# Kernel tuning notes

Measured on AMD Instinct MI355X. Metric: run time of the kernel, lower is better.

## Reference

```python
import jax, jax.numpy as jnp
import numpy as np

B = 8
N = 1024


def _sqrtm_psd(P):
    # symmetric PSD matrix square root via eigendecomposition
    w, V = jnp.linalg.eigh(P)
    return (V * jnp.sqrt(jnp.clip(w, 0.0))) @ V.T


def setup_inputs() -> dict:
    key = jax.random.key(0)
    k1, k2, k3 = jax.random.split(key, 3)
    x = jax.random.normal(k1, (1, B, N, 1), dtype=jnp.float32)
    # PSD covariance with nonnegative entries so abs() is a no-op and sqrtm is real
    A = jax.random.uniform(k2, (N, N), dtype=jnp.float32)
    P_u = (A @ A.T) / N
    Q_k = jax.random.uniform(k3, (N, N), dtype=jnp.float32)
    return {"x": x, "P_u": P_u, "Q_k": Q_k}


def reference(x, P_u, Q_k):
    n = x.shape[2]  # N
    # sigma = x.repeat(1,1,1,N): [1,B,N,N]
    sigma0 = jnp.broadcast_to(x, (1, x.shape[1], n, n))
    # p = sqrtm(N * |P_u|)
    p = _sqrtm_psd(n * jnp.abs(P_u))
    # concat(sigma+p, sigma-p) along last dim -> [1,B,N,2N]
    sigma = jnp.concatenate((sigma0 + p, sigma0 - p), axis=3)
    scale = 1.0 / (2 * n)
    x_bar = jnp.mean(sigma, axis=3)  # [1,B,N]
    # Faithful to original: only sigma[0,0] is used for the deviations,
    # while the mean varies with the batch index i2.
    points = sigma[0, 0]  # [N, 2N]
    c = points[None, :, :] - x_bar[0][:, :, None]  # [B, N, 2N]
    S = jnp.einsum('bni,bmi->bnm', c, c)  # sum of 2N outer products per batch
    P_k = S * scale + (Q_k ** 2) * 0.01
    return P_k, jnp.transpose(sigma, (0, 1, 3, 2))


if __name__ == "__main__":
    out = reference(**setup_inputs())
    print(out[0].shape, out[1].shape)
```

## Files before the change

kernel.cpp:

```cpp
#include <hip/hip_runtime.h>
#include <math.h>

#define NN 1024
#define BB 8
#define NS_ITERS 10
#define EPS_SHIFT 4.0f
#define MB (1u<<20)

typedef __attribute__((ext_vector_type(8))) short short8;
typedef __attribute__((ext_vector_type(4))) float floatx4;

__device__ __forceinline__ ushort f2bf(float f) {
    union { float f; uint32_t u; } v; v.f = f;
    uint32_t u = v.u;
    uint32_t r = (u + 0x7fffu + ((u >> 16) & 1u)) >> 16;
    return (ushort)r;
}
__device__ __forceinline__ float bf2f(ushort h) {
    union { uint32_t u; float f; } v; v.u = ((uint32_t)h) << 16;
    return v.f;
}

__device__ __forceinline__ void gload16(const ushort* g, ushort* s) {
    __builtin_amdgcn_global_load_lds(
        (__attribute__((address_space(1))) unsigned int*)(g),
        (__attribute__((address_space(3))) unsigned int*)(s), 16, 0, 0);
}

__device__ __forceinline__ float block_sum(float v) {
    #pragma unroll
    for (int off = 32; off > 0; off >>= 1) v += __shfl_down(v, off, 64);
    __shared__ float red[4];
    int lane = threadIdx.x & 63, wid = threadIdx.x >> 6;
    if (lane == 0) red[wid] = v;
    __syncthreads();
    float t = 0.f;
    if (threadIdx.x == 0) t = red[0] + red[1] + red[2] + red[3];
    return t;
}

__global__ __launch_bounds__(256) void matvec_abs(const float* __restrict__ pu,
                                                  const float* __restrict__ x,
                                                  float* __restrict__ y,
                                                  int use_ones) {
    int row = blockIdx.x;
    const float4* pr = (const float4*)(pu + (size_t)row * NN);
    float4 p = pr[threadIdx.x];
    float s;
    if (use_ones) {
        s = fabsf(p.x) + fabsf(p.y) + fabsf(p.z) + fabsf(p.w);
    } else {
        float4 xx = ((const float4*)x)[threadIdx.x];
        s = fabsf(p.x) * xx.x + fabsf(p.y) * xx.y + fabsf(p.z) * xx.z + fabsf(p.w) * xx.w;
    }
    s = block_sum(s);
    if (threadIdx.x == 0) y[row] = s;
}

__global__ void norm_vec(const float* __restrict__ y, float* __restrict__ v) {
    float ss = 0.f;
    for (int i = threadIdx.x; i < NN; i += 256) { float t = y[i]; ss += t * t; }
    #pragma unroll
    for (int off = 32; off > 0; off >>= 1) ss += __shfl_down(ss, off, 64);
    __shared__ float red[4];
    __shared__ float s_inv;
    int lane = threadIdx.x & 63, wid = threadIdx.x >> 6;
    if (lane == 0) red[wid] = ss;
    __syncthreads();
    if (threadIdx.x == 0) s_inv = rsqrtf(red[0] + red[1] + red[2] + red[3]);
    __syncthreads();
    float inv = s_inv;
    for (int i = threadIdx.x; i < NN; i += 256) v[i] = y[i] * inv;
}

__global__ void dot_vec(const float* __restrict__ a, const float* __restrict__ b,
                        float* __restrict__ out) {
    float s = 0.f;
    for (int i = threadIdx.x; i < NN; i += 256) s += a[i] * b[i];
    s = block_sum(s);
    if (threadIdx.x == 0) out[0] = s;
}

__global__ __launch_bounds__(256) void deflate_kernel(const float* __restrict__ pu,
                                                      const float* __restrict__ v,
                                                      const float* __restrict__ w,
                                                      float* __restrict__ sc,
                                                      float* __restrict__ D) {
    int idx = blockIdx.x * 256 + threadIdx.x;
    int row = idx >> 8;
    int c0 = (idx & 255) << 2;
    float lam = sc[5];
    float vr = v[row], wr = w[row];
    float4 p = ((const float4*)pu)[idx];
    float4 vc = *(const float4*)(v + c0);
    float4 wc = *(const float4*)(w + c0);
    float4 d;
    d.x = (float)NN * (fabsf(p.x) - vr * wc.x - wr * vc.x + lam * vr * vc.x);
    d.y = (float)NN * (fabsf(p.y) - vr * wc.y - wr * vc.y + lam * vr * vc.y);
    d.z = (float)NN * (fabsf(p.z) - vr * wc.z - wr * vc.z + lam * vr * vc.z);
    d.w = (float)NN * (fabsf(p.w) - vr * wc.w - wr * vc.w + lam * vr * vc.w);
    int dd = row - c0;
    if (dd == 0) d.x += EPS_SHIFT;
    else if (dd == 1) d.y += EPS_SHIFT;
    else if (dd == 2) d.z += EPS_SHIFT;
    else if (dd == 3) d.w += EPS_SHIFT;
    ((float4*)D)[idx] = d;
    float ss = d.x * d.x + d.y * d.y + d.z * d.z + d.w * d.w;
    ss = block_sum(ss);
    if (threadIdx.x == 0) atomicAdd(sc, ss);
}

__global__ void finalize_kernel(float* sc) {
    float c = sqrtf(sc[0]);
    sc[1] = 1.f / c;
    sc[2] = sqrtf(c);
    sc[4] = sqrtf((float)NN * sc[5]);
}

__device__ __forceinline__ void tile_swizzle64(int& row0, int& col0, int& zz) {
    int f = blockIdx.x + (blockIdx.y << 4) + (blockIdx.z << 8);
    int p = f & 7;
    int i = f >> 3;
    if (gridDim.z == 2) {
        zz = p & 1;
        int s = p >> 1;
        row0 = (((s >> 1) << 3) + (i >> 3)) << 6;
        col0 = (((s & 1) << 3) + (i & 7)) << 6;
    } else {
        zz = 0;
        row0 = (((p >> 1) << 2) + (i >> 3)) << 6;
        col0 = (((p & 1) << 3) + (i & 7)) << 6;
    }
}

__device__ __forceinline__ void mm_dev(const ushort* __restrict__ Ah,
                                       const ushort* __restrict__ Al,
                                       const ushort* __restrict__ Bh,
                                       const ushort* __restrict__ Bl,
                                       int row0, int col0, int kb, int kc,
                                       float* __restrict__ Cf,
                                       float* __restrict__ CfT,
                                       ushort* __restrict__ Chi,
                                       ushort* __restrict__ Clo) {
    __shared__ __align__(16) ushort lds[4 * 4 * 2048];
    const int t = threadIdx.x;
    const int w = t >> 6, l = t & 63;
    const int fm = l & 15, fq = l >> 4;
    const int lrow = l >> 2;
    const int lcol = (l & 3) << 3;

    const ushort* gh = w ? Bh : Ah;
    const ushort* gl = w ? Bl : Al;
    const int r0 = w ? col0 : row0;
    const ushort* ghp = gh + (size_t)(r0 + lrow) * NN + kb + lcol;
    const ushort* glp = gl + (size_t)(r0 + lrow) * NN + kb + lcol;

    floatx4 acc[4][2];
    #pragma unroll
    for (int mi = 0; mi < 4; ++mi) {
        acc[mi][0] = (floatx4)0.f;
        acc[mi][1] = (floatx4)0.f;
    }

    auto STAGE = [&](int bufi, int kt) {
        const int koff = kt << 5;
        ushort* sb = lds + (bufi << 13) + (w << 12);
        #pragma unroll
        for (int rb = 0; rb < 4; ++rb) {
            gload16(ghp + (size_t)(rb << 4) * NN + koff, sb + (rb << 9));
            gload16(glp + (size_t)(rb << 4) * NN + koff, sb + 2048 + (rb << 9));
        }
    };

    auto COMPUTE = [&](int bufi) {
        const ushort* Ash = lds + (bufi << 13);
        const ushort* Asl = Ash + 2048;
        const ushort* Bsh = Ash + 4096;
        const ushort* Bsl = Ash + 6144;
        const int bo = ((w << 5) + fm) * 32 + (fq << 3);
        short8 bh0 = *(const short8*)&Bsh[bo];
        short8 bh1 = *(const short8*)&Bsh[bo + 512];
        short8 bl0 = *(const short8*)&Bsl[bo];
        short8 bl1 = *(const short8*)&Bsl[bo + 512];
        #pragma unroll
        for (int mi = 0; mi < 4; ++mi) {
            const int ao = ((mi << 4) + fm) * 32 + (fq << 3);
            short8 ah = *(const short8*)&Ash[ao];
            short8 al = *(const short8*)&Asl[ao];
            acc[mi][0] = __builtin_amdgcn_mfma_f32_16x16x32_bf16(ah, bh0, acc[mi][0], 0, 0, 0);
            acc[mi][1] = __builtin_amdgcn_mfma_f32_16x16x32_bf16(ah, bh1, acc[mi][1], 0, 0, 0);
            acc[mi][0] = __builtin_amdgcn_mfma_f32_16x16x32_bf16(al, bh0, acc[mi][0], 0, 0, 0);
            acc[mi][1] = __builtin_amdgcn_mfma_f32_16x16x32_bf16(al, bh1, acc[mi][1], 0, 0, 0);
            acc[mi][0] = __builtin_amdgcn_mfma_f32_16x16x32_bf16(ah, bl0, acc[mi][0], 0, 0, 0);
            acc[mi][1] = __builtin_amdgcn_mfma_f32_16x16x32_bf16(ah, bl1, acc[mi][1], 0, 0, 0);
        }
    };

    const int nk = kc >> 5;
    STAGE(0, 0);
    STAGE(1, 1);
    STAGE(2, 2);
    #pragma unroll 1
    for (int kt = 0; kt < nk; ++kt) {
        if (kt + 2 < nk)       asm volatile("s_waitcnt vmcnt(16)" ::: "memory");
        else if (kt + 1 < nk)  asm volatile("s_waitcnt vmcnt(8)"  ::: "memory");
        else                   asm volatile("s_waitcnt vmcnt(0)"  ::: "memory");
        __builtin_amdgcn_s_barrier();
        __builtin_amdgcn_sched_barrier(0);
        if (kt + 3 < nk) STAGE((kt + 3) & 3, kt + 3);
        COMPUTE(kt & 3);
    }

    #pragma unroll
    for (int mi = 0; mi < 4; ++mi) {
        #pragma unroll
        for (int r = 0; r < 4; ++r) {
            int row = row0 + (mi << 4) + (fq << 2) + r;
            #pragma unroll
            for (int ni = 0; ni < 2; ++ni) {
                int col = col0 + (w << 5) + (ni << 4) + fm;
                float v = acc[mi][ni][r];
                size_t idx = (size_t)row * NN + col;
                if (Cf) {
                    Cf[idx] = v;
                } else {
                    ushort h = f2bf(v);
                    Chi[idx] = h;
                    Clo[idx] = f2bf(v - bf2f(h));
                }
            }
        }
    }

    if (CfT) {
        __syncthreads();
        float* lf = (float*)lds;
        #pragma unroll
        for (int mi = 0; mi < 4; ++mi) {
            #pragma unroll
            for (int r = 0; r < 4; ++r) {
                int rl = (mi << 4) + (fq << 2) + r;
                #pragma unroll
                for (int ni = 0; ni < 2; ++ni) {
                    int cl = (w << 5) + (ni << 4) + fm;
                    lf[cl * 68 + rl] = acc[mi][ni][r];
                }
            }
        }
        __syncthreads();
        int c = t >> 1, half = t & 1;
        const float* src = lf + c * 68 + (half << 5);
        float* dst = CfT + (size_t)(col0 + c) * NN + row0 + (half << 5);
        #pragma unroll
        for (int j = 0; j < 8; ++j)
            *(float4*)(dst + (j << 2)) = *(const float4*)(src + (j << 2));
    }
}

__global__ __launch_bounds__(128) void k_stage1(const ushort* __restrict__ Zh,
                                                const ushort* __restrict__ Zl,
                                                const ushort* __restrict__ Yh,
                                                const ushort* __restrict__ Yl,
                                                float* __restrict__ Mp,
                                                float* __restrict__ MpT0,
                                                float* __restrict__ MpT1) {
    int row0, col0, s;
    tile_swizzle64(row0, col0, s);
    mm_dev(Zh, Zl, Yh, Yl, row0, col0,
           s * (NN / 2), NN / 2, Mp + (size_t)s * NN * NN,
           s ? MpT1 : MpT0, nullptr, nullptr);
}

__global__ __launch_bounds__(128) void k_stage2(const ushort* __restrict__ Yh,
                                                const ushort* __restrict__ Yl,
                                                const ushort* __restrict__ Wh,
                                                const ushort* __restrict__ Wl,
                                                const ushort* __restrict__ Zh,
                                                const ushort* __restrict__ Zl,
                                                ushort* __restrict__ Ynh,
                                                ushort* __restrict__ Ynl,
                                                ushort* __restrict__ Znh,
                                                ushort* __restrict__ Znl) {
    int row0, col0, zz;
    tile_swizzle64(row0, col0, zz);
    if (zz == 0)
        mm_dev(Yh, Yl, Wh, Wl, row0, col0, 0, NN,
               nullptr, nullptr, Ynh, Ynl);
    else
        mm_dev(Wh, Wl, Zh, Zl, row0, col0, 0, NN,
               nullptr, nullptr, Znh, Znl);
}

__global__ __launch_bounds__(128) void k_final(const ushort* __restrict__ Yh,
                                               const ushort* __restrict__ Yl,
                                               const ushort* __restrict__ Wh,
                                               const ushort* __restrict__ Wl,
                                               float* __restrict__ Yf,
                                               float* __restrict__ YfT) {
    int row0, col0, zz;
    tile_swizzle64(row0, col0, zz);
    mm_dev(Yh, Yl, Wh, Wl, row0, col0, 0, NN,
           Yf, YfT, nullptr, nullptr);
}

__global__ __launch_bounds__(256) void k_wsplit(const float* __restrict__ Mp,
                                                const float* __restrict__ MpT0,
                                                const float* __restrict__ MpT1,
                                                ushort* __restrict__ Wh,
                                                ushort* __restrict__ Wl) {
    int i = blockIdx.x * 256 + threadIdx.x;
    int row = i >> 8, c0 = (i & 255) << 2;
    float4 m0 = ((const float4*)Mp)[i];
    float4 m1 = ((const float4*)Mp)[i + NN * NN / 4];
    float4 t0 = ((const float4*)MpT0)[i];
    float4 t1 = ((const float4*)MpT1)[i];
    float wv[4] = {-0.25f * (m0.x + m1.x + t0.x + t1.x),
                   -0.25f * (m0.y + m1.y + t0.y + t1.y),
                   -0.25f * (m0.z + m1.z + t0.z + t1.z),
                   -0.25f * (m0.w + m1.w + t0.w + t1.w)};
    int dd = row - c0;
    if (dd >= 0 && dd < 4) wv[dd] += 1.5f;
    ushort4 hv, lv;
    ushort* hp = (ushort*)&hv; ushort* lp = (ushort*)&lv;
    #pragma unroll
    for (int j = 0; j < 4; ++j) {
        ushort h = f2bf(wv[j]); hp[j] = h; lp[j] = f2bf(wv[j] - bf2f(h));
    }
    *(ushort4*)&Wh[(size_t)i << 2] = hv;
    *(ushort4*)&Wl[(size_t)i << 2] = lv;
}

__global__ __launch_bounds__(256) void k_wsplit0(const float* __restrict__ D,
                                                 const float* __restrict__ sc,
                                                 ushort* __restrict__ Yh,
                                                 ushort* __restrict__ Yl,
                                                 ushort* __restrict__ Wh,
                                                 ushort* __restrict__ Wl) {
    int i = blockIdx.x * 256 + threadIdx.x;
    int row = i >> 8, c0 = (i & 255) << 2;
    float invc = sc[1];
    float4 d = ((const float4*)D)[i];
    float yv[4] = {d.x * invc, d.y * invc, d.z * invc, d.w * invc};
    ushort4 yh, yl, wh, wl;
    ushort* yhp = (ushort*)&yh; ushort* ylp = (ushort*)&yl;
    ushort* whp = (ushort*)&wh; ushort* wlp = (ushort*)&wl;
    int dd = row - c0;
    #pragma unroll
    for (int j = 0; j < 4; ++j) {
        float y = yv[j];
        ushort h = f2bf(y); yhp[j] = h; ylp[j] = f2bf(y - bf2f(h));
        float wv = ((dd == j) ? 1.5f : 0.f) - 0.5f * y;
        ushort h2 = f2bf(wv); whp[j] = h2; wlp[j] = f2bf(wv - bf2f(h2));
    }
    *(ushort4*)&Yh[(size_t)i << 2] = yh;
    *(ushort4*)&Yl[(size_t)i << 2] = yl;
    *(ushort4*)&Wh[(size_t)i << 2] = wh;
    *(ushort4*)&Wl[(size_t)i << 2] = wl;
}

__global__ __launch_bounds__(256) void out0_kernel(const float* __restrict__ x,
                                                   const float* __restrict__ pu,
                                                   const float* __restrict__ qk,
                                                   float* __restrict__ out) {
    int i = blockIdx.x * blockDim.x + threadIdx.x;
    int rem = i & (NN * NN / 4 - 1);
    int b = i >> 18;
    int n = rem >> 8;
    int m4 = (rem & 255) << 2;
    float dn = x[n] - x[b * NN + n];
    float4 x0v = *(const float4*)(x + m4);
    float4 xbv = *(const float4*)(x + b * NN + m4);
    float4 pv = ((const float4*)pu)[rem];
    float4 qv = ((const float4*)qk)[rem];
    float4 o;
    o.x = dn * (x0v.x - xbv.x) + fabsf(pv.x) + 0.01f * qv.x * qv.x;
    o.y = dn * (x0v.y - xbv.y) + fabsf(pv.y) + 0.01f * qv.y * qv.y;
    o.z = dn * (x0v.z - xbv.z) + fabsf(pv.z) + 0.01f * qv.z * qv.z;
    o.w = dn * (x0v.w - xbv.w) + fabsf(pv.w) + 0.01f * qv.w * qv.w;
    ((float4*)out)[i] = o;
}

__global__ __launch_bounds__(256) void k_out1(const float* __restrict__ x,
                                              const float* __restrict__ Yf,
                                              const float* __restrict__ YfT,
                                              const float* __restrict__ sc,
                                              const float* __restrict__ v,
                                              float* __restrict__ out1) {
    int i = blockIdx.x * 256 + threadIdx.x;
    int j = i >> 8, i0 = (i & 255) << 2;
    float s = 0.5f * sc[2], s1v = sc[4] * v[j];
    float4 yr = *(const float4*)(Yf + (size_t)j * NN + i0);
    float4 yc = *(const float4*)(YfT + (size_t)j * NN + i0);
    float4 vc = *(const float4*)(v + i0);
    float4 p;
    p.x = s * (yr.x + yc.x) + s1v * vc.x;
    p.y = s * (yr.y + yc.y) + s1v * vc.y;
    p.z = s * (yr.z + yc.z) + s1v * vc.z;
    p.w = s * (yr.w + yc.w) + s1v * vc.w;
    #pragma unroll
    for (int b = 0; b < BB; ++b) {
        float4 xv = *(const float4*)(x + b * NN + i0);
        float4 a, m;
        a.x = xv.x + p.x; a.y = xv.y + p.y; a.z = xv.z + p.z; a.w = xv.w + p.w;
        m.x = xv.x - p.x; m.y = xv.y - p.y; m.z = xv.z - p.z; m.w = xv.w - p.w;
        float* base = out1 + (size_t)b * 2 * NN * NN;
        *(float4*)(base + (size_t)j * NN + i0) = a;
        *(float4*)(base + (size_t)(NN + j) * NN + i0) = m;
    }
}

extern "C" void kernel_launch(void* const* d_in, const int* in_sizes, int n_in,
                              void* d_out, int out_size, void* d_ws, size_t ws_size,
                              hipStream_t stream) {
    const float* x  = (const float*)d_in[0];
    const float* pu = (const float*)d_in[1];
    const float* qk = (const float*)d_in[2];
    float* out = (float*)d_out;
    char* ws = (char*)d_ws;

    float* Mp = (float*)ws;
    float* D  = Mp;
    float* Yf = Mp;
    float* YfT = (float*)(ws + (size_t)4 * MB);
    ushort* hi[5]; ushort* lo[5];
    for (int k = 0; k < 5; ++k) {
        hi[k] = (ushort*)(ws + (size_t)8 * MB + (size_t)k * 4 * MB);
        lo[k] = (ushort*)(ws + (size_t)8 * MB + (size_t)k * 4 * MB + 2 * MB);
    }
    float* vv = (float*)(ws + (size_t)28 * MB);
    float* vw = (float*)(ws + (size_t)28 * MB + 4096);
    float* vt = (float*)(ws + (size_t)28 * MB + 8192);
    float* sc = (float*)(ws + (size_t)28 * MB + 12288);

    hipMemsetAsync(sc, 0, 64, stream);
    matvec_abs<<<NN, 256, 0, stream>>>(pu, vv, vt, 1);
    norm_vec<<<1, 256, 0, stream>>>(vt, vv);
    matvec_abs<<<NN, 256, 0, stream>>>(pu, vv, vt, 0);
    norm_vec<<<1, 256, 0, stream>>>(vt, vv);
    matvec_abs<<<NN, 256, 0, stream>>>(pu, vv, vw, 0);
    dot_vec<<<1, 256, 0, stream>>>(vv, vw, sc + 5);
    deflate_kernel<<<NN * NN / 4 / 256, 256, 0, stream>>>(pu, vv, vw, sc, D);
    finalize_kernel<<<1, 1, 0, stream>>>(sc);

    k_wsplit0<<<NN * NN / 4 / 256, 256, 0, stream>>>(D, sc, hi[0], lo[0], hi[1], lo[1]);
    k_stage2<<<dim3(16, 16, 1), 128, 0, stream>>>(hi[0], lo[0], hi[1], lo[1],
                                                  hi[0], lo[0],
                                                  hi[2], lo[2], hi[3], lo[3]);
    int Y = 2, Z = 1, f0 = 0, f1 = 3, f2 = 4;

    for (int it = 1; it < NS_ITERS; ++it) {
        int W = f0;
        float* MpT0 = (float*)hi[f1];
        float* MpT1 = (float*)hi[f2];
        k_stage1<<<dim3(16, 16, 2), 128, 0, stream>>>(hi[Z], lo[Z], hi[Y], lo[Y],
                                                      Mp, MpT0, MpT1);
        k_wsplit<<<NN * NN / 4 / 256, 256, 0, stream>>>(Mp, MpT0, MpT1,
                                                        hi[W], lo[W]);
        if (it + 1 < NS_ITERS) {
            int Yn = f1, Zn = f2;
            k_stage2<<<dim3(16, 16, 2), 128, 0, stream>>>(
                hi[Y], lo[Y], hi[W], lo[W], hi[Z], lo[Z],
                hi[Yn], lo[Yn], hi[Zn], lo[Zn]);
            f0 = Y; f1 = Z; f2 = W;
            Y = Yn; Z = Zn;
        } else {
            k_final<<<dim3(16, 16, 1), 128, 0, stream>>>(hi[Y], lo[Y], hi[W], lo[W],
                                                         Yf, YfT);
        }
    }

    out0_kernel<<<(BB * NN * NN / 4) / 256, 256, 0, stream>>>(x, pu, qk, out);
    k_out1<<<NN * NN / 4 / 256, 256, 0, stream>>>(x, Yf, YfT, sc, vv,
                                                  out + (size_t)BB * NN * NN);
}
```

Before: 569.3 us.

## Split K across the two waves in the tile GEMM and reduce through LDS

The 64x64 tile GEMM used to split the output columns between its two waves, with both waves sharing every staged K-slice behind a block barrier. Now each wave computes the full 64x64 tile over alternating K-slices with its own private staging and no per-iteration barrier, and the two partial sums are added through LDS at the end. This removes the per-step s_barrier and lets each wave pipeline on its own. In exchange each wave holds twice as many accumulators, needs more registers, and adds an LDS reduction epilogue, which may lower occupancy.

```diff
diff --git a/kernel.cpp b/kernel.cpp
--- a/kernel.cpp
+++ b/kernel.cpp
@@ -142,83 +142,107 @@
                                        float* __restrict__ CfT,
                                        ushort* __restrict__ Chi,
                                        ushort* __restrict__ Clo) {
-    __shared__ __align__(16) ushort lds[4 * 4 * 2048];
+    __shared__ __align__(16) ushort lds[4 * 8192];
     const int t = threadIdx.x;
     const int w = t >> 6, l = t & 63;
     const int fm = l & 15, fq = l >> 4;
     const int lrow = l >> 2;
     const int lcol = (l & 3) << 3;
 
-    const ushort* gh = w ? Bh : Ah;
-    const ushort* gl = w ? Bl : Al;
-    const int r0 = w ? col0 : row0;
-    const ushort* ghp = gh + (size_t)(r0 + lrow) * NN + kb + lcol;
-    const ushort* glp = gl + (size_t)(r0 + lrow) * NN + kb + lcol;
-
-    floatx4 acc[4][2];
-    #pragma unroll
-    for (int mi = 0; mi < 4; ++mi) {
-        acc[mi][0] = (floatx4)0.f;
-        acc[mi][1] = (floatx4)0.f;
-    }
-
-    auto STAGE = [&](int bufi, int kt) {
+    const ushort* Ahp = Ah + (size_t)(row0 + lrow) * NN + kb + lcol;
+    const ushort* Alp = Al + (size_t)(row0 + lrow) * NN + kb + lcol;
+    const ushort* Bhp = Bh + (size_t)(col0 + lrow) * NN + kb + lcol;
+    const ushort* Blp = Bl + (size_t)(col0 + lrow) * NN + kb + lcol;
+
+    floatx4 acc[4][4];
+    #pragma unroll
+    for (int mi = 0; mi < 4; ++mi)
+        #pragma unroll
+        for (int ni = 0; ni < 4; ++ni) acc[mi][ni] = (floatx4)0.f;
+
+    auto STAGE = [&](int kt) {
         const int koff = kt << 5;
-        ushort* sb = lds + (bufi << 13) + (w << 12);
+        ushort* sb = lds + ((kt & 3) << 13);
         #pragma unroll
         for (int rb = 0; rb < 4; ++rb) {
-            gload16(ghp + (size_t)(rb << 4) * NN + koff, sb + (rb << 9));
-            gload16(glp + (size_t)(rb << 4) * NN + koff, sb + 2048 + (rb << 9));
+            gload16(Ahp + (size_t)(rb << 4) * NN + koff, sb + (rb << 9));
+            gload16(Alp + (size_t)(rb << 4) * NN + koff, sb + 2048 + (rb << 9));
+            gload16(Bhp + (size_t)(rb << 4) * NN + koff, sb + 4096 + (rb << 9));
+            gload16(Blp + (size_t)(rb << 4) * NN + koff, sb + 6144 + (rb << 9));
         }
     };
 
-    auto COMPUTE = [&](int bufi) {
-        const ushort* Ash = lds + (bufi << 13);
+    const int nk = kc >> 5;
+    STAGE(w);
+    STAGE(w + 2);
+    #pragma unroll 1
+    for (int kt = w; kt < nk; kt += 2) {
+        if (kt + 2 < nk) asm volatile("s_waitcnt vmcnt(16)" ::: "memory");
+        else             asm volatile("s_waitcnt vmcnt(0)"  ::: "memory");
+        __builtin_amdgcn_sched_barrier(0);
+        const ushort* Ash = lds + ((kt & 3) << 13);
         const ushort* Asl = Ash + 2048;
         const ushort* Bsh = Ash + 4096;
         const ushort* Bsl = Ash + 6144;
-        const int bo = ((w << 5) + fm) * 32 + (fq << 3);
-        short8 bh0 = *(const short8*)&Bsh[bo];
-        short8 bh1 = *(const short8*)&Bsh[bo + 512];
-        short8 bl0 = *(const short8*)&Bsl[bo];
-        short8 bl1 = *(const short8*)&Bsl[bo + 512];
-        #pragma unroll
-        for (int mi = 0; mi < 4; ++mi) {
-            const int ao = ((mi << 4) + fm) * 32 + (fq << 3);
-            short8 ah = *(const short8*)&Ash[ao];
-            short8 al = *(const short8*)&Asl[ao];
-            acc[mi][0] = __builtin_amdgcn_mfma_f32_16x16x32_bf16(ah, bh0, acc[mi][0], 0, 0, 0);
-            acc[mi][1] = __builtin_amdgcn_mfma_f32_16x16x32_bf16(ah, bh1, acc[mi][1], 0, 0, 0);
-            acc[mi][0] = __builtin_amdgcn_mfma_f32_16x16x32_bf16(al, bh0, acc[mi][0], 0, 0, 0);
-            acc[mi][1] = __builtin_amdgcn_mfma_f32_16x16x32_bf16(al, bh1, acc[mi][1], 0, 0, 0);
-            acc[mi][0] = __builtin_amdgcn_mfma_f32_16x16x32_bf16(ah, bl0, acc[mi][0], 0, 0, 0);
-            acc[mi][1] = __builtin_amdgcn_mfma_f32_16x16x32_bf16(ah, bl1, acc[mi][1], 0, 0, 0);
+        short8 ah[4], al[4], bh[4], bl[4];
+        #pragma unroll
+        for (int i = 0; i < 4; ++i) {
+            const int ro = ((i << 4) + fm) * 32 + (fq << 3);
+            ah[i] = *(const short8*)&Ash[ro];
+            al[i] = *(const short8*)&Asl[ro];
+            bh[i] = *(const short8*)&Bsh[ro];
+            bl[i] = *(const short8*)&Bsl[ro];
         }
-    };
-
-    const int nk = kc >> 5;
-    STAGE(0, 0);
-    STAGE(1, 1);
-    STAGE(2, 2);
-    #pragma unroll 1
-    for (int kt = 0; kt < nk; ++kt) {
-        if (kt + 2 < nk)       asm volatile("s_waitcnt vmcnt(16)" ::: "memory");
-        else if (kt + 1 < nk)  asm volatile("s_waitcnt vmcnt(8)"  ::: "memory");
-        else                   asm volatile("s_waitcnt vmcnt(0)"  ::: "memory");
-        __builtin_amdgcn_s_barrier();
+        asm volatile("s_waitcnt lgkmcnt(0)" ::: "memory");
         __builtin_amdgcn_sched_barrier(0);
-        if (kt + 3 < nk) STAGE((kt + 3) & 3, kt + 3);
-        COMPUTE(kt & 3);
-    }
-
-    #pragma unroll
-    for (int mi = 0; mi < 4; ++mi) {
+        if (kt + 4 < nk) STAGE(kt + 4);
+        #pragma unroll
+        for (int mi = 0; mi < 4; ++mi)
+            #pragma unroll
+            for (int ni = 0; ni < 4; ++ni) {
+                acc[mi][ni] = __builtin_amdgcn_mfma_f32_16x16x32_bf16(ah[mi], bh[ni], acc[mi][ni], 0, 0, 0);
+                acc[mi][ni] = __builtin_amdgcn_mfma_f32_16x16x32_bf16(al[mi], bh[ni], acc[mi][ni], 0, 0, 0);
+                acc[mi][ni] = __builtin_amdgcn_mfma_f32_16x16x32_bf16(ah[mi], bl[ni], acc[mi][ni], 0, 0, 0);
+            }
+    }
+
+    __syncthreads();
+    float* lf = (float*)lds;
+    const int dep0 = w ? 0 : 2;
+    const int own0 = w ? 2 : 0;
+    #pragma unroll
+    for (int m2 = 0; m2 < 2; ++m2) {
+        #pragma unroll
+        for (int ni = 0; ni < 4; ++ni)
+            #pragma unroll
+            for (int r = 0; r < 4; ++r) {
+                int row = ((dep0 + m2) << 4) + (fq << 2) + r;
+                int col = (ni << 4) + fm;
+                lf[row * 66 + col] = acc[dep0 + m2][ni][r];
+            }
+    }
+    __syncthreads();
+    #pragma unroll
+    for (int m2 = 0; m2 < 2; ++m2) {
+        #pragma unroll
+        for (int ni = 0; ni < 4; ++ni)
+            #pragma unroll
+            for (int r = 0; r < 4; ++r) {
+                int row = ((own0 + m2) << 4) + (fq << 2) + r;
+                int col = (ni << 4) + fm;
+                acc[own0 + m2][ni][r] += lf[row * 66 + col];
+            }
+    }
+
+    #pragma unroll
+    for (int m2 = 0; m2 < 2; ++m2) {
+        const int mi = own0 + m2;
         #pragma unroll
         for (int r = 0; r < 4; ++r) {
             int row = row0 + (mi << 4) + (fq << 2) + r;
             #pragma unroll
-            for (int ni = 0; ni < 2; ++ni) {
-                int col = col0 + (w << 5) + (ni << 4) + fm;
+            for (int ni = 0; ni < 4; ++ni) {
+                int col = col0 + (ni << 4) + fm;
                 float v = acc[mi][ni][r];
                 size_t idx = (size_t)row * NN + col;
                 if (Cf) {
@@ -234,15 +258,15 @@
 
     if (CfT) {
         __syncthreads();
-        float* lf = (float*)lds;
-        #pragma unroll
-        for (int mi = 0; mi < 4; ++mi) {
+        #pragma unroll
+        for (int m2 = 0; m2 < 2; ++m2) {
+            const int mi = own0 + m2;
             #pragma unroll
             for (int r = 0; r < 4; ++r) {
                 int rl = (mi << 4) + (fq << 2) + r;
                 #pragma unroll
-                for (int ni = 0; ni < 2; ++ni) {
-                    int cl = (w << 5) + (ni << 4) + fm;
+                for (int ni = 0; ni < 4; ++ni) {
+                    int cl = (ni << 4) + fm;
                     lf[cl * 68 + rl] = acc[mi][ni][r];
                 }
             }
```

Result: slower. 700.8 us (+23.1%).
